# Kernel tuning notes

Hardware: AMD Instinct MI355X
Metric: run time of the kernel (lower is better)

Reference implementation:

```python
import jax, jax.numpy as jnp
import numpy as np

# Hamilton product tables: out component q uses weight IDX[q,p] with sign SGN[q,p]
# applied to input component p. Components order: (r, i, j, k); weights order: (rr, ri, rj, rk).
IDX = np.array([[0, 1, 2, 3], [1, 0, 3, 2], [2, 3, 0, 1], [3, 2, 1, 0]])
SGN = np.array([[1., -1., -1., -1.], [1., 1., 1., -1.], [1., -1., 1., 1.], [1., 1., -1., 1.]], dtype=np.float32)


def _qlinear(x4, w, b):
    # x4: (B, 4, Cin4, H, W); w: (4, Cout4, Cin4); b: (4, Cout4)
    # Quaternion 1x1 conv == channel-mixing matmul with Hamilton sign structure.
    wstk = jnp.asarray(SGN)[:, :, None, None] * w[IDX]  # (4,4,Cout4,Cin4)
    out = jnp.einsum('qpoc,bpchw->bqohw', wstk, x4)
    return out + b[None, :, :, None, None]


def _qdwconv(x4, w, b):
    # x4: (B, 4, Cc, H, W); w: (4, Cc, 1, 3, 3) depthwise per-channel; b: (4, Cc)
    Cc = x4.shape[2]
    comps = [x4[:, p] for p in range(4)]  # each (B, Cc, H, W)
    outs = []
    for qc in range(4):
        acc = None
        for p in range(4):
            c = SGN[qc, p] * jax.lax.conv_general_dilated(
                comps[p], w[IDX[qc, p]], window_strides=(1, 1), padding='SAME',
                feature_group_count=Cc, dimension_numbers=('NCHW', 'OIHW', 'NCHW'))
            acc = c if acc is None else acc + c
        outs.append(acc + b[qc][None, :, None, None])
    return jnp.stack(outs, axis=1)  # (B, 4, Cc, H, W)


def setup_inputs() -> dict:
    key = jax.random.key(0)
    ks = jax.random.split(key, 4)
    B, Cc, H, W = 8, 256, 32, 32   # dim = 4*Cc = 1024
    dim = 4 * Cc
    num_heads, key_dim = 8, 128
    h = 3 * num_heads * key_dim    # 3072 total -> 768 per component
    x = jax.random.normal(ks[0], (B, Cc, 4, H, W), jnp.float32)
    w_qkv = jax.random.normal(ks[1], (4, h // 4, dim // 4), jnp.float32) * (1.0 / np.sqrt(dim))
    b_qkv = jnp.zeros((4, h // 4), jnp.float32)
    w_proj = jax.random.normal(ks[2], (4, dim // 4, dim // 4), jnp.float32) * (1.0 / np.sqrt(dim))
    b_proj = jnp.zeros((4, dim // 4), jnp.float32)
    w_pe = jax.random.normal(ks[3], (4, dim // 4, 1, 3, 3), jnp.float32) * (1.0 / 6.0)
    b_pe = jnp.zeros((4, dim // 4), jnp.float32)
    return {'x': x, 'w_qkv': w_qkv, 'b_qkv': b_qkv, 'w_proj': w_proj,
            'b_proj': b_proj, 'w_pe': w_pe, 'b_pe': b_pe}


def reference(x, w_qkv, b_qkv, w_proj, b_proj, w_pe, b_pe):
    B, Cc, Q, H, W = x.shape
    num_heads, key_dim = 8, 128
    scale = key_dim ** -0.5
    N = H * W
    xq = jnp.transpose(x, (0, 2, 1, 3, 4))            # (B, 4, Cc, H, W)
    qkv = _qlinear(xq, w_qkv, b_qkv)                  # (B, 4, 768, H, W)
    q4, k4, v4 = jnp.split(qkv, 3, axis=2)            # each (B, 4, 256, H, W)

    def to_heads(t):  # (B,4,Cc,H,W) -> (B, heads, key_dim, N)
        return t.reshape(B, 4 * Cc, N).reshape(B, num_heads, key_dim, N)

    q, k, v = to_heads(q4), to_heads(k4), to_heads(v4)
    scores = jnp.einsum('bhdn,bhdm->bhnm', q, k) * scale   # (B,H,N,N) fully materialized
    attn = jax.nn.softmax(scores, axis=-1)
    out = jnp.einsum('bhnm,bhdm->bhdn', attn, v)           # (B,H,key_dim,N)
    out4 = out.reshape(B, 4, Cc, H, W)
    out = _qlinear(out4, w_proj, b_proj) + _qdwconv(xq, w_pe, b_pe)
    return jnp.transpose(out, (0, 2, 1, 3, 4))             # (B, Cc, 4, H, W)
```

## Files before the change

### kernel.cpp

```cpp
#include <hip/hip_runtime.h>
#include <hip/hip_bf16.h>

typedef unsigned short u16;
typedef float f32x4 __attribute__((ext_vector_type(4)));
typedef __bf16 bf16x8 __attribute__((ext_vector_type(8)));
typedef __bf16 bf16x4 __attribute__((ext_vector_type(4)));
typedef unsigned short su8v __attribute__((ext_vector_type(8)));
typedef unsigned short su4v __attribute__((ext_vector_type(4)));
typedef short s16x4 __attribute__((ext_vector_type(4)));

#define BB 8
#define NHD 8
#define DD 128
#define NN 1024
#define DIM 1024
#define H3 3072
#define MM 8192
#define QSC (0.08838834764831845f * 1.4426950408889634f)

__constant__ int   d_IDX[16] = {0,1,2,3, 1,0,3,2, 2,3,0,1, 3,2,1,0};
__constant__ float d_SGN[16] = {1.f,-1.f,-1.f,-1.f, 1.f,1.f,1.f,-1.f,
                                1.f,-1.f,1.f,1.f,  1.f,1.f,-1.f,1.f};

__device__ __forceinline__ f32x4 mfma16(su8v a, su8v b, f32x4 c) {
  return __builtin_amdgcn_mfma_f32_16x16x32_bf16(
      __builtin_bit_cast(bf16x8, a), __builtin_bit_cast(bf16x8, b), c, 0, 0, 0);
}
__device__ __forceinline__ f32x4 mfma16h(su4v a, su4v b, f32x4 c) {
#if __has_builtin(__builtin_amdgcn_mfma_f32_16x16x16_bf16)
  return __builtin_amdgcn_mfma_f32_16x16x16_bf16(
      __builtin_bit_cast(bf16x4, a), __builtin_bit_cast(bf16x4, b), c, 0, 0, 0);
#elif __has_builtin(__builtin_amdgcn_mfma_f32_16x16x16bf16_1k)
  return __builtin_amdgcn_mfma_f32_16x16x16bf16_1k(
      __builtin_bit_cast(s16x4, a), __builtin_bit_cast(s16x4, b), c, 0, 0, 0);
#else
  f32x4 d = c;
  asm("v_mfma_f32_16x16x16_bf16 %0, %1, %2, %0" : "+v"(d) : "v"(a), "v"(b));
  return d;
#endif
}
__device__ __forceinline__ u16 f2b(float f) {
  unsigned int u = __builtin_bit_cast(unsigned int, f);
  u += 0x7fffu + ((u >> 16) & 1u);
  return (u16)(u >> 16);
}
__device__ __forceinline__ float b2f(u16 v) {
  unsigned int u = ((unsigned int)v) << 16;
  return __builtin_bit_cast(float, u);
}
typedef const __attribute__((address_space(1))) unsigned int* gas_t;
typedef __attribute__((address_space(3))) unsigned int* las_t;
__device__ __forceinline__ void gll16(const u16* g, u16* l) {
  __builtin_amdgcn_global_load_lds((gas_t)g, (las_t)l, 16, 0, 0);
}

__global__ __launch_bounds__(256) void prep_weff(
    const float* __restrict__ wqkv, const float* __restrict__ wproj,
    u16* __restrict__ weffQ, u16* __restrict__ weffP) {
  int tid = blockIdx.x * 256 + threadIdx.x;
  int stride = gridDim.x * 256;
  for (int i = tid; i < H3 * DIM; i += stride) {
    int row = i >> 10, col = i & 1023;
    int q = row / 768, o = row - q * 768;
    int p = col >> 8, c = col & 255;
    float v = d_SGN[q * 4 + p] * wqkv[(d_IDX[q * 4 + p] * 768 + o) * 256 + c];
    if (o < 256) v *= QSC;
    weffQ[i] = f2b(v);
  }
  for (int i = tid; i < DIM * DIM; i += stride) {
    int row = i >> 10, col = i & 1023;
    int q = row >> 8, o = row & 255;
    int p = col >> 8, c = col & 255;
    weffP[i] = f2b(d_SGN[q * 4 + p] * wproj[(d_IDX[q * 4 + p] * 256 + o) * 256 + c]);
  }
}

__global__ __launch_bounds__(256) void prep_x(
    const float* __restrict__ x, u16* __restrict__ Ax) {
  __shared__ u16 T[64 * 264];
  int blk = blockIdx.x;
  int nc = blk & 15;
  int cc = (blk >> 4) & 3;
  int b = blk >> 6;
  int n0 = nc * 64, c0 = cc * 64;
  int tid = threadIdx.x;
  int nseg = tid & 15, rq = tid >> 4;
#pragma unroll
  for (int pass = 0; pass < 16; ++pass) {
    int rr = pass * 16 + rq;
    int p = rr >> 6, c = rr & 63;
    float4 f = *(const float4*)(x + (((size_t)(b * 256 + c0 + c)) * 4 + p) * 1024 +
                                n0 + nseg * 4);
    T[(nseg * 4 + 0) * 264 + rr] = f2b(f.x);
    T[(nseg * 4 + 1) * 264 + rr] = f2b(f.y);
    T[(nseg * 4 + 2) * 264 + rr] = f2b(f.z);
    T[(nseg * 4 + 3) * 264 + rr] = f2b(f.w);
  }
  __syncthreads();
  int nl = tid >> 5, lc = tid & 31;
#pragma unroll
  for (int pass = 0; pass < 8; ++pass) {
    int n = pass * 8 + nl;
    su8v v = *(const su8v*)(&T[n * 264 + lc * 8]);
    int pcl = lc * 8;
    *(su8v*)(Ax + (size_t)(b * 1024 + n0 + n) * 1024 + (pcl >> 6) * 256 + c0 +
             (pcl & 63)) = v;
  }
}

template <int BM, int BN>
__device__ __forceinline__ void gemm_core8(
    const u16* __restrict__ Ag, const u16* __restrict__ Bg,
    u16* As, u16* Bs, int tid, f32x4 (&acc)[4][4]) {
  constexpr int WN = BN / 64;
  constexpr int AC = BM / 64;
  constexpr int BC = BN / 64;
  constexpr int NT = 16;
  int w = tid >> 6, lane = tid & 63, l16 = lane & 15, quad = lane >> 4;
  int wm = w / WN, wn = w % WN;
  int x7 = l16 & 7;
  int srow = lane >> 3;
  int sblk = (lane & 7) ^ srow;

  auto STAGE_A = [&](int tt, int bs) {
#pragma unroll
    for (int c = 0; c < AC; ++c) {
      int r0 = c * 64 + w * 8;
      gll16(Ag + (size_t)(r0 + srow) * 1024 + tt * 64 + sblk * 8,
            As + (size_t)bs * (BM * 64) + r0 * 64);
    }
  };
  auto STAGE_B = [&](int tt, int bs) {
#pragma unroll
    for (int c = 0; c < BC; ++c) {
      int r0 = c * 64 + w * 8;
      gll16(Bg + (size_t)(r0 + srow) * 1024 + tt * 64 + sblk * 8,
            Bs + (size_t)bs * (BN * 64) + r0 * 64);
    }
  };

  STAGE_A(0, 0); STAGE_B(0, 0);
  STAGE_A(1, 1); STAGE_B(1, 1);
  asm volatile("s_waitcnt vmcnt(6)" ::: "memory");
  __builtin_amdgcn_s_barrier();

  int cur = 0, nxt = 1, stg = 2;
  for (int t = 0; t < NT; ++t) {
    const u16* At = As + (size_t)cur * (BM * 64);
    const u16* Bt = Bs + (size_t)cur * (BN * 64);
#pragma unroll
    for (int kk = 0; kk < 2; ++kk) {
      su8v af[4], bf[4];
#pragma unroll
      for (int i = 0; i < 4; ++i)
        af[i] = *(const su8v*)(At + (wm * 64 + i * 16 + l16) * 64 +
                               ((kk * 4 + quad) ^ x7) * 8);
#pragma unroll
      for (int j = 0; j < 4; ++j)
        bf[j] = *(const su8v*)(Bt + (wn * 64 + j * 16 + l16) * 64 +
                               ((kk * 4 + quad) ^ x7) * 8);
      if (t + 2 < NT) {
        if (kk == 0) STAGE_A(t + 2, stg);
        else         STAGE_B(t + 2, stg);
      }
      __builtin_amdgcn_s_setprio(1);
#pragma unroll
      for (int i = 0; i < 4; ++i)
#pragma unroll
        for (int j = 0; j < 4; ++j)
          acc[i][j] = mfma16(af[i], bf[j], acc[i][j]);
      __builtin_amdgcn_s_setprio(0);
    }
    if (t < NT - 2)       asm volatile("s_waitcnt vmcnt(6)" ::: "memory");
    else if (t == NT - 2) asm volatile("s_waitcnt vmcnt(0)" ::: "memory");
    asm volatile("" ::: "memory");
    __builtin_amdgcn_s_barrier();
    asm volatile("" ::: "memory");
    int tmp = cur; cur = nxt; nxt = stg; stg = tmp;
  }
}

__global__ __launch_bounds__(512, 2) void gemm_qkv_mfma(
    const u16* __restrict__ Ax, const u16* __restrict__ weffQ,
    const float* __restrict__ bqkv,
    u16* __restrict__ Qb, u16* __restrict__ Kb, u16* __restrict__ VbT) {
  __shared__ u16 smem[3 * 384 * 64];
  int bn0 = blockIdx.x * 256;
  int col0 = blockIdx.y * 128;
  int q = col0 / 768;
  int off = col0 - q * 768;
  int sel = off >> 8;
  int head = (q * 256 + (off & 255)) >> 7;
  int tid = threadIdx.x;
  int w = tid >> 6, lane = tid & 63, l16 = lane & 15, quad = lane >> 4;
  f32x4 acc[4][4];
#pragma unroll
  for (int i = 0; i < 4; ++i)
#pragma unroll
    for (int j = 0; j < 4; ++j) acc[i][j] = (f32x4){0.f, 0.f, 0.f, 0.f};

  if (sel == 2) {
    gemm_core8<256, 128>(Ax + (size_t)bn0 * 1024, weffQ + (size_t)col0 * 1024,
                         smem, smem + 3 * 256 * 64, tid, acc);
    int wm = w >> 1, wn = w & 1;
#pragma unroll
    for (int j = 0; j < 4; ++j) {
      int dl = wn * 64 + j * 16 + l16;
      float bias = bqkv[col0 + dl];
#pragma unroll
      for (int i = 0; i < 4; ++i) {
        int m = bn0 + wm * 64 + i * 16 + quad * 4;
        int b = m >> 10, npos = m & 1023;
        int bh = b * NHD + head;
        su4v pk;
#pragma unroll
        for (int r = 0; r < 4; ++r) pk[r] = f2b(acc[i][j][r] + bias);
        *(su4v*)(VbT + ((size_t)bh * DD + dl) * NN + npos) = pk;
      }
    }
  } else {
    gemm_core8<128, 256>(weffQ + (size_t)col0 * 1024, Ax + (size_t)bn0 * 1024,
                         smem, smem + 3 * 128 * 64, tid, acc);
    int wm = w >> 2, wn = w & 3;
    u16* dst = (sel == 0) ? Qb : Kb;
    float sc = (sel == 0) ? (float)QSC : 1.0f;
#pragma unroll
    for (int i = 0; i < 4; ++i) {
      int dbase = wm * 64 + i * 16 + quad * 4;
      float4 b4 = *(const float4*)(bqkv + col0 + dbase);
#pragma unroll
      for (int j = 0; j < 4; ++j) {
        int n = bn0 + wn * 64 + j * 16 + l16;
        int b = n >> 10, npos = n & 1023;
        int bh = b * NHD + head;
        su4v pk;
        pk[0] = f2b(acc[i][j][0] + b4.x * sc);
        pk[1] = f2b(acc[i][j][1] + b4.y * sc);
        pk[2] = f2b(acc[i][j][2] + b4.z * sc);
        pk[3] = f2b(acc[i][j][3] + b4.w * sc);
        *(su4v*)(dst + ((size_t)bh * NN + npos) * DD + dbase) = pk;
      }
    }
  }
}

__global__ __launch_bounds__(256) void attn_mfma(
    const u16* __restrict__ Qb, const u16* __restrict__ Kb,
    const u16* __restrict__ VbT, u16* __restrict__ OP,
    float* __restrict__ LS) {
  __shared__ u16 Ks[64 * 128];
  __shared__ u16 Vt[128 * 64];
  int blk = blockIdx.x;
  int bh = blk & 63;
  int rest = blk >> 6;
  int qt = rest & 7;
  int half = rest >> 3;
  int n0 = qt * 128;
  int tid = threadIdx.x;
  int w = tid >> 6, lane = tid & 63, l16 = lane & 15, quad = lane >> 4;
  const u16* Qg = Qb + ((size_t)bh * NN + n0) * DD;
  const u16* Kg = Kb + (size_t)bh * NN * DD;
  const u16* Vg = VbT + (size_t)bh * DD * NN;
  int x7 = l16 & 7;

  su8v qreg[2][4];
#pragma unroll
  for (int mi = 0; mi < 2; ++mi)
#pragma unroll
    for (int ch = 0; ch < 4; ++ch)
      qreg[mi][ch] = *(const su8v*)(Qg + (size_t)(w * 32 + mi * 16 + l16) * DD +
                                    ch * 32 + quad * 8);

  float ls[2] = {0.f, 0.f};
  f32x4 accO[2][8];
#pragma unroll
  for (int mi = 0; mi < 2; ++mi)
#pragma unroll
    for (int dt = 0; dt < 8; ++dt) accO[mi][dt] = (f32x4){0.f, 0.f, 0.f, 0.f};

  for (int kt = 0; kt < 8; ++kt) {
    int c0 = half * 512 + kt * 64;
    __syncthreads();
#pragma unroll
    for (int t = 0; t < 4; ++t) {
      int ci = w * 4 + t;
      int krow = ci * 4 + (lane >> 4);
      int kblk = (lane & 15) ^ (krow & 7);
      gll16(Kg + (size_t)(c0 + krow) * DD + kblk * 8, Ks + ci * 512);
      int dv = ci * 8 + (lane >> 3);
      int vblk = (lane & 7) ^ (dv & 7);
      gll16(Vg + (size_t)dv * NN + c0 + vblk * 8, Vt + ci * 512);
    }
    __syncthreads();

#pragma unroll
    for (int j = 0; j < 4; ++j) {
      f32x4 s0 = (f32x4){0.f, 0.f, 0.f, 0.f};
      f32x4 s1 = (f32x4){0.f, 0.f, 0.f, 0.f};
#pragma unroll
      for (int ch = 0; ch < 4; ++ch) {
        su8v kf = *(const su8v*)(Ks + (j * 16 + l16) * 128 +
                                 (((ch * 4 + quad) ^ x7) * 8));
        s0 = mfma16(kf, qreg[0][ch], s0);
        s1 = mfma16(kf, qreg[1][ch], s1);
      }
      su4v p0, p1;
#pragma unroll
      for (int r = 0; r < 4; ++r) {
        float pa = __builtin_exp2f(s0[r]);
        ls[0] += pa;
        p0[r] = (u16)(__builtin_bit_cast(unsigned int, pa) >> 16);
        float pb = __builtin_exp2f(s1[r]);
        ls[1] += pb;
        p1[r] = (u16)(__builtin_bit_cast(unsigned int, pb) >> 16);
      }
#pragma unroll
      for (int dt = 0; dt < 8; ++dt) {
        su4v vf = *(const su4v*)(Vt + (dt * 16 + l16) * 64 +
                                 ((((j * 2 + (quad >> 1)) ^ x7) << 3) +
                                  (quad & 1) * 4));
        accO[0][dt] = mfma16h(p0, vf, accO[0][dt]);
        accO[1][dt] = mfma16h(p1, vf, accO[1][dt]);
      }
    }
  }

#pragma unroll
  for (int mi = 0; mi < 2; ++mi) {
    float s = ls[mi];
    s += __shfl_xor(s, 16, 64);
    s += __shfl_xor(s, 32, 64);
    ls[mi] = s;
  }
  size_t hb = (size_t)(half * 64 + bh);
  if (quad == 0) {
#pragma unroll
    for (int mi = 0; mi < 2; ++mi)
      LS[hb * NN + n0 + w * 32 + mi * 16 + l16] = ls[mi];
  }
#pragma unroll
  for (int mi = 0; mi < 2; ++mi)
#pragma unroll
    for (int r = 0; r < 4; ++r) {
      int row = w * 32 + mi * 16 + quad * 4 + r;
      size_t base = (hb * NN + n0 + row) * DD;
#pragma unroll
      for (int dt = 0; dt < 8; ++dt)
        OP[base + dt * 16 + l16] = f2b(accO[mi][dt][r]);
    }
}

__global__ __launch_bounds__(256) void attn_merge(
    const u16* __restrict__ OP, const float* __restrict__ LS,
    u16* __restrict__ AO) {
  size_t idx = (size_t)blockIdx.x * 256 + threadIdx.x;
  size_t e = idx * 4;
  int d = (int)(e & 127);
  size_t bhn = e >> 7;
  su4v a = *(const su4v*)(OP + bhn * DD + d);
  su4v b = *(const su4v*)(OP + (size_t)64 * NN * DD + bhn * DD + d);
  float inv = 1.0f / (LS[bhn] + LS[bhn + 64 * NN]);
  int bh = (int)(bhn >> 10), n = (int)(bhn & 1023);
  int bb = bh >> 3, head = bh & 7;
  su4v o;
#pragma unroll
  for (int r = 0; r < 4; ++r) o[r] = f2b((b2f(a[r]) + b2f(b[r])) * inv);
  *(su4v*)(AO + ((size_t)(bb * 1024 + n) * 1024) + head * 128 + d) = o;
}

__global__ __launch_bounds__(256) void qdwconv_kernel(
    const float* __restrict__ x, const float* __restrict__ wpe,
    const float* __restrict__ bpe, float* __restrict__ pe) {
  int blk = blockIdx.x;
  int co = blk & 255;
  int b = blk >> 8;
  __shared__ float pl[4][34 * 34];
  __shared__ float wsm[4][9];
  int tid = threadIdx.x;
  for (int i = tid; i < 4 * 34 * 34; i += 256) ((float*)pl)[i] = 0.f;
  if (tid < 36) wsm[tid / 9][tid % 9] = wpe[((tid / 9) * 256 + co) * 9 + tid % 9];
  __syncthreads();
  for (int i = tid; i < 4 * 1024; i += 256) {
    int p = i >> 10, n = i & 1023;
    int h = n >> 5, ww = n & 31;
    pl[p][(h + 1) * 34 + (ww + 1)] =
        x[(((size_t)b * 256 + co) * 4 + p) * 1024 + n];
  }
  __syncthreads();
  for (int n = tid; n < 1024; n += 256) {
    int h = n >> 5, ww = n & 31;
    float in[4][9];
#pragma unroll
    for (int p = 0; p < 4; ++p)
#pragma unroll
      for (int t = 0; t < 9; ++t)
        in[p][t] = pl[p][(h + t / 3) * 34 + (ww + t % 3)];
#pragma unroll
    for (int q = 0; q < 4; ++q) {
      float acc = bpe[q * 256 + co];
#pragma unroll
      for (int p = 0; p < 4; ++p) {
        int idx = d_IDX[q * 4 + p];
        float s = d_SGN[q * 4 + p];
        float sub = 0.f;
#pragma unroll
        for (int t = 0; t < 9; ++t) sub += in[p][t] * wsm[idx][t];
        acc += s * sub;
      }
      pe[(((size_t)b * 256 + co) * 4 + q) * 1024 + n] = acc;
    }
  }
}

__global__ __launch_bounds__(512, 2) void gemm_proj_mfma(
    const u16* __restrict__ AO, const u16* __restrict__ weffP,
    const float* __restrict__ bproj, const float* __restrict__ pe,
    float* __restrict__ out) {
  __shared__ u16 smem[3 * 384 * 64];
  int n0 = blockIdx.x * 256;
  int m0 = blockIdx.y * 128;
  int tid = threadIdx.x;
  f32x4 acc[4][4];
#pragma unroll
  for (int i = 0; i < 4; ++i)
#pragma unroll
    for (int j = 0; j < 4; ++j) acc[i][j] = (f32x4){0.f, 0.f, 0.f, 0.f};
  gemm_core8<128, 256>(weffP + (size_t)m0 * 1024, AO + (size_t)n0 * 1024,
                       smem, smem + 3 * 128 * 64, tid, acc);

  int w = tid >> 6, lane = tid & 63, l16 = lane & 15, quad = lane >> 4;
  int wm = w >> 2, wn = w & 3;
#pragma unroll
  for (int i = 0; i < 4; ++i) {
#pragma unroll
    for (int r = 0; r < 4; ++r) {
      int mrow = m0 + wm * 64 + i * 16 + quad * 4 + r;
      int q = mrow >> 8, o = mrow & 255;
      float bias = bproj[mrow];
#pragma unroll
      for (int j = 0; j < 4; ++j) {
        int n = n0 + wn * 64 + j * 16 + l16;
        int b = n >> 10, npos = n & 1023;
        size_t oidx = (((size_t)b * 256 + o) * 4 + q) * 1024 + npos;
        out[oidx] = pe[oidx] + acc[i][j][r] + bias;
      }
    }
  }
}

extern "C" void kernel_launch(void* const* d_in, const int* in_sizes, int n_in,
                              void* d_out, int out_size, void* d_ws,
                              size_t ws_size, hipStream_t stream) {
  const float* x      = (const float*)d_in[0];
  const float* w_qkv  = (const float*)d_in[1];
  const float* b_qkv  = (const float*)d_in[2];
  const float* w_proj = (const float*)d_in[3];
  const float* b_proj = (const float*)d_in[4];
  const float* w_pe   = (const float*)d_in[5];
  const float* b_pe   = (const float*)d_in[6];
  float* out = (float*)d_out;

  u16* ws = (u16*)d_ws;
  u16* weffQ = ws;
  u16* weffP = weffQ + (size_t)H3 * DIM;
  u16* Ax    = weffP + (size_t)DIM * DIM;
  u16* Qb    = Ax + (size_t)MM * DIM;
  u16* Kb    = Qb + (size_t)BB * NHD * NN * DD;
  u16* VbT   = Kb + (size_t)BB * NHD * NN * DD;
  u16* AO    = VbT + (size_t)BB * NHD * DD * NN;
  float* PE  = (float*)(AO + (size_t)MM * DIM);
  u16* OP    = (u16*)(PE + (size_t)MM * DIM);
  float* LS  = (float*)(OP + (size_t)2 * 64 * NN * DD);

  hipLaunchKernelGGL(prep_weff, dim3(4096), dim3(256), 0, stream,
                     w_qkv, w_proj, weffQ, weffP);
  hipLaunchKernelGGL(prep_x, dim3(512), dim3(256), 0, stream, x, Ax);
  hipLaunchKernelGGL(gemm_qkv_mfma, dim3(MM / 256, H3 / 128), dim3(512), 0,
                     stream, Ax, weffQ, b_qkv, Qb, Kb, VbT);
  hipLaunchKernelGGL(attn_mfma, dim3(1024), dim3(256), 0, stream,
                     Qb, Kb, VbT, OP, LS);
  hipLaunchKernelGGL(attn_merge, dim3((64 * NN * DD) / (256 * 4)), dim3(256),
                     0, stream, OP, LS, AO);
  hipLaunchKernelGGL(qdwconv_kernel, dim3(BB * 256), dim3(256), 0, stream,
                     x, w_pe, b_pe, PE);
  hipLaunchKernelGGL(gemm_proj_mfma, dim3(MM / 256, DIM / 128), dim3(512), 0,
                     stream, AO, weffP, b_proj, PE, out);
}
```

Baseline: 288.8 us.

## Widen LDS swizzles for K and V tiles and compute softmax row sums via MFMA

The K tile swizzle now XORs with the full 16-row index instead of 8, and the V^T global layout gets a half-swap on npos so the 4-element V fragment reads land in different LDS banks. Both changes target LDS bank conflicts in the attention inner loop. The per-lane exp2 row-sum accumulation and its final cross-lane shuffle reduction are replaced by an extra MFMA of P against a vector of bf16 ones. This adds two MFMAs per j iteration, and the row sums are now taken over the bf16-truncated probabilities rather than the fp32 values.

```diff
diff --git a/kernel.cpp b/kernel.cpp
--- a/kernel.cpp
+++ b/kernel.cpp
@@ -207,6 +207,7 @@
     for (int j = 0; j < 4; ++j) {
       int dl = wn * 64 + j * 16 + l16;
       float bias = bqkv[col0 + dl];
+      int hswap = ((dl >> 3) & 1) << 2;
 #pragma unroll
       for (int i = 0; i < 4; ++i) {
         int m = bn0 + wm * 64 + i * 16 + quad * 4;
@@ -215,7 +216,7 @@
         su4v pk;
 #pragma unroll
         for (int r = 0; r < 4; ++r) pk[r] = f2b(acc[i][j][r] + bias);
-        *(su4v*)(VbT + ((size_t)bh * DD + dl) * NN + npos) = pk;
+        *(su4v*)(VbT + ((size_t)bh * DD + dl) * NN + (npos ^ hswap)) = pk;
       }
     }
   } else {
@@ -262,6 +263,7 @@
   const u16* Kg = Kb + (size_t)bh * NN * DD;
   const u16* Vg = VbT + (size_t)bh * DD * NN;
   int x7 = l16 & 7;
+  int vhalf = ((quad & 1) ^ (l16 >> 3)) * 4;
 
   su8v qreg[2][4];
 #pragma unroll
@@ -271,7 +273,11 @@
       qreg[mi][ch] = *(const su8v*)(Qg + (size_t)(w * 32 + mi * 16 + l16) * DD +
                                     ch * 32 + quad * 8);
 
-  float ls[2] = {0.f, 0.f};
+  su4v ones;
+  ones[0] = 0x3F80; ones[1] = 0x3F80; ones[2] = 0x3F80; ones[3] = 0x3F80;
+  f32x4 accL[2];
+  accL[0] = (f32x4){0.f, 0.f, 0.f, 0.f};
+  accL[1] = (f32x4){0.f, 0.f, 0.f, 0.f};
   f32x4 accO[2][8];
 #pragma unroll
   for (int mi = 0; mi < 2; ++mi)
@@ -285,7 +291,7 @@
     for (int t = 0; t < 4; ++t) {
       int ci = w * 4 + t;
       int krow = ci * 4 + (lane >> 4);
-      int kblk = (lane & 15) ^ (krow & 7);
+      int kblk = (lane & 15) ^ (krow & 15);
       gll16(Kg + (size_t)(c0 + krow) * DD + kblk * 8, Ks + ci * 512);
       int dv = ci * 8 + (lane >> 3);
       int vblk = (lane & 7) ^ (dv & 7);
@@ -300,7 +306,7 @@
 #pragma unroll
       for (int ch = 0; ch < 4; ++ch) {
         su8v kf = *(const su8v*)(Ks + (j * 16 + l16) * 128 +
-                                 (((ch * 4 + quad) ^ x7) * 8));
+                                 (((ch * 4 + quad) ^ l16) * 8));
         s0 = mfma16(kf, qreg[0][ch], s0);
         s1 = mfma16(kf, qreg[1][ch], s1);
       }
@@ -308,35 +314,28 @@
 #pragma unroll
       for (int r = 0; r < 4; ++r) {
         float pa = __builtin_exp2f(s0[r]);
-        ls[0] += pa;
         p0[r] = (u16)(__builtin_bit_cast(unsigned int, pa) >> 16);
         float pb = __builtin_exp2f(s1[r]);
-        ls[1] += pb;
         p1[r] = (u16)(__builtin_bit_cast(unsigned int, pb) >> 16);
       }
+      accL[0] = mfma16h(p0, ones, accL[0]);
+      accL[1] = mfma16h(p1, ones, accL[1]);
 #pragma unroll
       for (int dt = 0; dt < 8; ++dt) {
         su4v vf = *(const su4v*)(Vt + (dt * 16 + l16) * 64 +
-                                 ((((j * 2 + (quad >> 1)) ^ x7) << 3) +
-                                  (quad & 1) * 4));
+                                 ((((j * 2 + (quad >> 1)) ^ x7) << 3) + vhalf));
         accO[0][dt] = mfma16h(p0, vf, accO[0][dt]);
         accO[1][dt] = mfma16h(p1, vf, accO[1][dt]);
       }
     }
   }
 
-#pragma unroll
-  for (int mi = 0; mi < 2; ++mi) {
-    float s = ls[mi];
-    s += __shfl_xor(s, 16, 64);
-    s += __shfl_xor(s, 32, 64);
-    ls[mi] = s;
-  }
   size_t hb = (size_t)(half * 64 + bh);
-  if (quad == 0) {
+  if (l16 == 0) {
 #pragma unroll
     for (int mi = 0; mi < 2; ++mi)
-      LS[hb * NN + n0 + w * 32 + mi * 16 + l16] = ls[mi];
+      *(float4*)(&LS[hb * NN + n0 + w * 32 + mi * 16 + quad * 4]) =
+          *(float4*)(&accL[mi]);
   }
 #pragma unroll
   for (int mi = 0; mi < 2; ++mi)
```

Result: no change. 290.1 us (+0.5%).
